# Kernel tuning notes

Hardware: AMD Instinct MI355X
Metric: run time of the kernel (lower is better)

Reference implementation:

```python
import jax, jax.numpy as jnp
import numpy as np

KPS = 39
EPS = 1e-05

def _prelu(h, a):
    return jnp.where(h >= 0, h, a * h)

def _ln(h, alpha, beta):
    mean = jnp.mean(h, axis=-1, keepdims=True)
    var = jnp.mean((h - mean) ** 2, axis=-1, keepdims=True)
    return (h - mean) / jnp.sqrt(var + EPS) * alpha + beta

def setup_inputs() -> dict:
    key = jax.random.key(0)
    ks = jax.random.split(key, 8)
    B, T = 256, 2048
    d_in, d_hid = 2 * KPS, 5 * KPS  # 78, 195
    # xavier_uniform with gain for relu = sqrt(2)
    def xavier(k, shape):
        fan_out, fan_in = shape
        gain = np.sqrt(2.0)
        bound = gain * np.sqrt(6.0 / (fan_in + fan_out))
        return jax.random.uniform(k, shape, jnp.float32, -bound, bound)
    return {
        "x": jax.random.normal(ks[0], (B, T, KPS), jnp.float32),
        "y": jax.random.normal(ks[1], (B, T, KPS), jnp.float32),
        "W1": xavier(ks[2], (d_hid, d_in)),   # [195, 78]
        "b1": jnp.zeros((d_hid,), jnp.float32),
        "W2": xavier(ks[3], (d_in, d_hid)),   # [78, 195]
        "b2": jnp.zeros((d_in,), jnp.float32),
        "a1": jnp.full((1,), 0.25, jnp.float32),  # PReLU default
        "a2": jnp.full((1,), 0.25, jnp.float32),
        "alpha1": jnp.ones((d_hid,), jnp.float32),
        "beta1": jnp.zeros((d_hid,), jnp.float32),
        "alpha2": jnp.ones((d_in,), jnp.float32),
        "beta2": jnp.zeros((d_in,), jnp.float32),
    }

def reference(x, y, W1, b1, W2, b2, a1, a2, alpha1, beta1, alpha2, beta2):
    joined = jnp.concatenate((x, y), axis=-1)        # [B, T, 78]
    h = jnp.einsum('btd,hd->bth', joined, W1) + b1   # [B, T, 195]
    h = _ln(_prelu(h, a1), alpha1, beta1)
    # dropout p=0.1 is identity in eval mode
    h = jnp.einsum('bth,dh->btd', h, W2) + b2        # [B, T, 78]
    h = _ln(_prelu(h, a2), alpha2, beta2)
    out = h + joined
    return out[..., :KPS], out[..., KPS:]
```

## Files before the change

kernel.cpp:

```cpp
#include <hip/hip_runtime.h>
#include <hip/hip_bf16.h>

typedef unsigned short u16;
typedef unsigned int   u32;

#define KPS     39
#define DIN     78
#define DHID    195
#define NTOKTOT (256*2048)

#define S1      104
#define S2      232
#define M1T     13
#define K1S     3
#define M2T     5
#define K2S     7
#define NW      8
#define TPI     (NW*16)
#define TPB     2048
#define NIT     (TPB/TPI)
#define NBLK    (NTOKTOT/TPB)

#define W1F_E (M1T*K1S*64*8)
#define W2F_E (M2T*K2S*64*8)
#define JND_E (TPI*S1)
#define HN_E  (TPI*S2)
#define SMEM_BYTES ((W1F_E+W2F_E+JND_E+HN_E)*2 + DIN*2*4 + DIN*4)

typedef __attribute__((ext_vector_type(8))) short short8;
typedef __attribute__((ext_vector_type(4))) float float4v;

static __device__ __forceinline__ u16 f2b(float v) {
  __hip_bfloat16 b = __float2bfloat16(v);
  return __builtin_bit_cast(u16, b);
}
static __device__ __forceinline__ float b2f(u16 u) {
  return __builtin_bit_cast(float, ((u32)u) << 16);
}

extern "C" __global__ __launch_bounds__(512, 2)
void fused_mlp_kernel(const float* __restrict__ xp,  const float* __restrict__ yp,
                      const float* __restrict__ W1p, const float* __restrict__ b1p,
                      const float* __restrict__ W2p, const float* __restrict__ b2p,
                      const float* __restrict__ a1p, const float* __restrict__ a2p,
                      const float* __restrict__ al1p,const float* __restrict__ be1p,
                      const float* __restrict__ al2p,const float* __restrict__ be2p,
                      float* __restrict__ out0, float* __restrict__ out1)
{
  extern __shared__ char smem[];
  u16*   W1F = (u16*)smem;
  u16*   W2F = W1F + W1F_E;
  u16*   JND = W2F + W2F_E;
  u16*   HN  = JND + JND_E;
  float* AB2 = (float*)(HN + HN_E);
  float* B2C = AB2 + DIN*2;

  const int tid  = threadIdx.x;
  const int lane = tid & 63;
  const int w    = tid >> 6;
  const int c    = lane & 15;
  const int quad = lane >> 4;
  const int wr   = w * 16;
  const int blockTok = blockIdx.x * TPB;

  float4v xr0, xr1, xr2, yr0, yr1, yr2;
  {
    const float4v* xw = (const float4v*)(xp + (size_t)(blockTok + wr) * KPS);
    const float4v* yw = (const float4v*)(yp + (size_t)(blockTok + wr) * KPS);
    xr0 = xw[lane];      yr0 = yw[lane];
    xr1 = xw[lane + 64]; yr1 = yw[lane + 64];
    if (lane < 28) { xr2 = xw[lane + 128]; yr2 = yw[lane + 128]; }
    else { xr2 = (float4v)0.f; yr2 = (float4v)0.f; }
  }

  {
    float* SCR = (float*)JND;
    if (tid < DIN*4) {
      int d = tid >> 2, p = tid & 3;
      float s = (p == 0) ? b2p[d] : 0.f;
      const float* wrow = W2p + d*DHID;
      for (int j = p; j < DHID; j += 4) s = __builtin_fmaf(wrow[j], be1p[j], s);
      SCR[tid] = s;
    }
  }
  __syncthreads();
  if (tid < DIN) {
    const float* SCR = (const float*)JND;
    B2C[tid] = SCR[4*tid] + SCR[4*tid+1] + SCR[4*tid+2] + SCR[4*tid+3];
    AB2[2*tid+0] = al2p[tid];
    AB2[2*tid+1] = be2p[tid];
  }
  for (int s = tid; s < M1T*K1S*64; s += 512) {
    int m = s/(K1S*64), r = s - m*(K1S*64);
    int kt = r >> 6, l = r & 63;
    int cc = l & 15, qq = l >> 4;
    int row = m*16 + cc, k0 = kt*32 + qq*8;
    short8 v;
    #pragma unroll
    for (int e = 0; e < 8; ++e) {
      int k = k0 + e; float f = 0.f;
      if (row < DHID) { if (k < DIN) f = W1p[row*DIN + k]; else if (k == DIN) f = b1p[row]; }
      v[e] = (short)f2b(f);
    }
    *(short8*)&W1F[(size_t)s*8] = v;
  }
  __syncthreads();
  for (int s = tid; s < M2T*K2S*64; s += 512) {
    int m = s/(K2S*64), r = s - m*(K2S*64);
    int kt = r >> 6, l = r & 63;
    int cc = l & 15, qq = l >> 4;
    int d = m*16 + cc, k0 = kt*32 + qq*8;
    short8 v;
    #pragma unroll
    for (int e = 0; e < 8; ++e) {
      int k = k0 + e; float f = 0.f;
      if (d < DIN) {
        if (k < DHID)       f = W2p[d*DHID + k] * al1p[k];
        else if (k == DHID) f = B2C[d];
      }
      v[e] = (short)f2b(f);
    }
    *(short8*)&W2F[(size_t)s*8] = v;
  }
  for (int i = tid; i < TPI*18; i += 512) {
    int t = i/18, cf = i - t*18;
    JND[t*S1 + DIN + cf] = (cf == 0) ? (u16)0x3F80 : (u16)0;
  }
  for (int i = tid; i < TPI*29; i += 512) {
    int t = i/29, cf = i - t*29;
    HN[t*S2 + DHID + cf] = (cf == 0) ? (u16)0x3F80 : (u16)0;
  }
  __syncthreads();

  const float a1v = a1p[0];
  const float a2v = a2p[0];

  int joff[12];
  #pragma unroll
  for (int s = 0; s < 3; ++s) {
    int i4 = lane + s*64;
    #pragma unroll
    for (int k = 0; k < 4; ++k) {
      int idx = i4*4 + k;
      int t = idx / KPS, cc2 = idx - t*KPS;
      joff[s*4+k] = (wr + t)*S1 + cc2;
    }
  }

  const u16* pW1 = W1F + (size_t)lane*8;
  const u16* pW2 = W2F + (size_t)lane*8;
  u16* pJ = JND + (wr + c)*S1;
  u16* pH = HN  + (wr + c)*S2;

  #pragma unroll 1
  for (int it = 0; it < NIT; ++it) {
    const int tb = blockTok + it * TPI;

    #pragma unroll
    for (int k = 0; k < 4; ++k) {
      JND[joff[k]]         = f2b(xr0[k]);
      JND[joff[k] + KPS]   = f2b(yr0[k]);
      JND[joff[4+k]]       = f2b(xr1[k]);
      JND[joff[4+k] + KPS] = f2b(yr1[k]);
    }
    if (lane < 28) {
      #pragma unroll
      for (int k = 0; k < 4; ++k) {
        JND[joff[8+k]]       = f2b(xr2[k]);
        JND[joff[8+k] + KPS] = f2b(yr2[k]);
      }
    }

    if (it + 1 < NIT) {
      const float4v* xw = (const float4v*)(xp + (size_t)(tb + TPI + wr) * KPS);
      const float4v* yw = (const float4v*)(yp + (size_t)(tb + TPI + wr) * KPS);
      xr0 = xw[lane];      yr0 = yw[lane];
      xr1 = xw[lane + 64]; yr1 = yw[lane + 64];
      if (lane < 28) { xr2 = xw[lane + 128]; yr2 = yw[lane + 128]; }
    }

    float4v acc1[M1T];
    #pragma unroll
    for (int m = 0; m < M1T; ++m)
      #pragma unroll
      for (int q = 0; q < 4; ++q) acc1[m][q] = 0.f;

    #pragma unroll
    for (int kt = 0; kt < K1S; ++kt) {
      short8 bfr = *(const short8*)&pJ[kt*32 + quad*8];
      #pragma unroll
      for (int m = 0; m < M1T; ++m) {
        short8 afr = *(const short8*)&pW1[(m*K1S + kt)*512];
        acc1[m] = __builtin_amdgcn_mfma_f32_16x16x32_bf16(afr, bfr, acc1[m], 0, 0, 0);
      }
    }

    float sum = 0.f, ss = 0.f;
    #pragma unroll
    for (int m = 0; m < M1T; ++m)
      #pragma unroll
      for (int q = 0; q < 4; ++q) {
        float h = acc1[m][q];
        float p = fmaxf(h, 0.f) + a1v * fminf(h, 0.f);
        acc1[m][q] = p;
        sum += p;
        ss = __builtin_fmaf(p, p, ss);
      }
    sum += __shfl_xor(sum, 16, 64);
    sum += __shfl_xor(sum, 32, 64);
    ss  += __shfl_xor(ss,  16, 64);
    ss  += __shfl_xor(ss,  32, 64);
    const float mean = sum * (1.f/DHID);
    const float istd = rsqrtf(ss*(1.f/DHID) - mean*mean + 1e-5f);

    #pragma unroll
    for (int m = 0; m < M1T; ++m) {
      int jb = m*16 + quad*4;
      if (m < 12) {
        ushort4 pk;
        pk.x = f2b((acc1[m][0] - mean)*istd);
        pk.y = f2b((acc1[m][1] - mean)*istd);
        pk.z = f2b((acc1[m][2] - mean)*istd);
        pk.w = f2b((acc1[m][3] - mean)*istd);
        *(ushort4*)&pH[jb] = pk;
      } else if (quad == 0) {
        pH[192] = f2b((acc1[m][0] - mean)*istd);
        pH[193] = f2b((acc1[m][1] - mean)*istd);
        pH[194] = f2b((acc1[m][2] - mean)*istd);
      }
    }

    float4v acc2[M2T];
    #pragma unroll
    for (int m = 0; m < M2T; ++m)
      #pragma unroll
      for (int q = 0; q < 4; ++q) acc2[m][q] = 0.f;

    #pragma unroll
    for (int kt = 0; kt < K2S; ++kt) {
      short8 bfr = *(const short8*)&pH[kt*32 + quad*8];
      #pragma unroll
      for (int m = 0; m < M2T; ++m) {
        short8 afr = *(const short8*)&pW2[(m*K2S + kt)*512];
        acc2[m] = __builtin_amdgcn_mfma_f32_16x16x32_bf16(afr, bfr, acc2[m], 0, 0, 0);
      }
    }

    float sum2 = 0.f, ss2 = 0.f;
    #pragma unroll
    for (int m = 0; m < M2T; ++m)
      #pragma unroll
      for (int q = 0; q < 4; ++q) {
        float h = acc2[m][q];
        float p = fmaxf(h, 0.f) + a2v * fminf(h, 0.f);
        acc2[m][q] = p;
        sum2 += p;
        ss2 = __builtin_fmaf(p, p, ss2);
      }
    sum2 += __shfl_xor(sum2, 16, 64);
    sum2 += __shfl_xor(sum2, 32, 64);
    ss2  += __shfl_xor(ss2,  16, 64);
    ss2  += __shfl_xor(ss2,  32, 64);
    const float mean2 = sum2 * (1.f/DIN);
    const float istd2 = rsqrtf(ss2*(1.f/DIN) - mean2*mean2 + 1e-5f);

    const int gt = tb + wr + c;
    #pragma unroll
    for (int m = 0; m < M2T; ++m) {
      int d0 = m*16 + quad*4;
      if (d0 < DIN) {
        ushort4 res = *(const ushort4*)&pJ[d0];
        u16 rr[4] = {res.x, res.y, res.z, res.w};
        #pragma unroll
        for (int r = 0; r < 4; ++r) {
          int d = d0 + r;
          if (d < DIN) {
            float2 ab = *(const float2*)&AB2[2*d];
            float  v  = (acc2[m][r] - mean2)*istd2*ab.x + ab.y + b2f(rr[r]);
            if (d < KPS) out0[(size_t)gt*KPS + d]         = v;
            else         out1[(size_t)gt*KPS + (d - KPS)] = v;
          }
        }
      }
    }
  }
}

extern "C" void kernel_launch(void* const* d_in, const int* in_sizes, int n_in,
                              void* d_out, int out_size, void* d_ws, size_t ws_size,
                              hipStream_t stream) {
  const float* xp   = (const float*)d_in[0];
  const float* yp   = (const float*)d_in[1];
  const float* W1p  = (const float*)d_in[2];
  const float* b1p  = (const float*)d_in[3];
  const float* W2p  = (const float*)d_in[4];
  const float* b2p  = (const float*)d_in[5];
  const float* a1p  = (const float*)d_in[6];
  const float* a2p  = (const float*)d_in[7];
  const float* al1p = (const float*)d_in[8];
  const float* be1p = (const float*)d_in[9];
  const float* al2p = (const float*)d_in[10];
  const float* be2p = (const float*)d_in[11];

  float* out0 = (float*)d_out;
  float* out1 = out0 + (size_t)NTOKTOT * KPS;

  hipFuncSetAttribute((const void*)fused_mlp_kernel,
                      hipFuncAttributeMaxDynamicSharedMemorySize, SMEM_BYTES);

  fused_mlp_kernel<<<NBLK, 512, SMEM_BYTES, stream>>>(
      xp, yp, W1p, b1p, W2p, b2p, a1p, a2p, al1p, be1p, al2p, be2p, out0, out1);
}
```

Measured before the change: 363.1 us.

## Feed GEMM2 B operand from registers, drop HN LDS buffer, double warps

Removes the HN shared-memory staging of the normalized hidden activations. The W2 fragment layout is permuted along K so the MFMA accumulator output of GEMM1 can be packed directly in registers as the B operand of GEMM2, saving an LDS write/read round trip per iteration. The freed LDS is used to raise the block from 8 to 16 waves (1024 threads) with launch bounds of 4. This raises occupancy but may increase register pressure from the packed array, and the preamble and synchronization now span a larger block.

```diff
diff --git a/kernel.cpp b/kernel.cpp
--- a/kernel.cpp
+++ b/kernel.cpp
@@ -10,12 +10,12 @@
 #define NTOKTOT (256*2048)
 
 #define S1      104
-#define S2      232
 #define M1T     13
 #define K1S     3
 #define M2T     5
 #define K2S     7
-#define NW      8
+#define NW      16
+#define NTHR    1024
 #define TPI     (NW*16)
 #define TPB     2048
 #define NIT     (TPB/TPI)
@@ -24,11 +24,11 @@
 #define W1F_E (M1T*K1S*64*8)
 #define W2F_E (M2T*K2S*64*8)
 #define JND_E (TPI*S1)
-#define HN_E  (TPI*S2)
-#define SMEM_BYTES ((W1F_E+W2F_E+JND_E+HN_E)*2 + DIN*2*4 + DIN*4)
+#define SMEM_BYTES ((W1F_E+W2F_E+JND_E)*2 + DIN*2*4 + DIN*4)
 
 typedef __attribute__((ext_vector_type(8))) short short8;
 typedef __attribute__((ext_vector_type(4))) float float4v;
+typedef __attribute__((ext_vector_type(4))) u32   uint4v;
 
 static __device__ __forceinline__ u16 f2b(float v) {
   __hip_bfloat16 b = __float2bfloat16(v);
@@ -38,7 +38,7 @@
   return __builtin_bit_cast(float, ((u32)u) << 16);
 }
 
-extern "C" __global__ __launch_bounds__(512, 2)
+extern "C" __global__ __launch_bounds__(NTHR, 4)
 void fused_mlp_kernel(const float* __restrict__ xp,  const float* __restrict__ yp,
                       const float* __restrict__ W1p, const float* __restrict__ b1p,
                       const float* __restrict__ W2p, const float* __restrict__ b2p,
@@ -51,8 +51,7 @@
   u16*   W1F = (u16*)smem;
   u16*   W2F = W1F + W1F_E;
   u16*   JND = W2F + W2F_E;
-  u16*   HN  = JND + JND_E;
-  float* AB2 = (float*)(HN + HN_E);
+  float* AB2 = (float*)(JND + JND_E);
   float* B2C = AB2 + DIN*2;
 
   const int tid  = threadIdx.x;
@@ -90,7 +89,7 @@
     AB2[2*tid+0] = al2p[tid];
     AB2[2*tid+1] = be2p[tid];
   }
-  for (int s = tid; s < M1T*K1S*64; s += 512) {
+  for (int s = tid; s < M1T*K1S*64; s += NTHR) {
     int m = s/(K1S*64), r = s - m*(K1S*64);
     int kt = r >> 6, l = r & 63;
     int cc = l & 15, qq = l >> 4;
@@ -105,15 +104,16 @@
     *(short8*)&W1F[(size_t)s*8] = v;
   }
   __syncthreads();
-  for (int s = tid; s < M2T*K2S*64; s += 512) {
+  for (int s = tid; s < M2T*K2S*64; s += NTHR) {
     int m = s/(K2S*64), r = s - m*(K2S*64);
     int kt = r >> 6, l = r & 63;
     int cc = l & 15, qq = l >> 4;
-    int d = m*16 + cc, k0 = kt*32 + qq*8;
+    int d = m*16 + cc;
     short8 v;
     #pragma unroll
     for (int e = 0; e < 8; ++e) {
-      int k = k0 + e; float f = 0.f;
+      int k = kt*32 + (e>>2)*16 + qq*4 + (e&3);
+      float f = 0.f;
       if (d < DIN) {
         if (k < DHID)       f = W2p[d*DHID + k] * al1p[k];
         else if (k == DHID) f = B2C[d];
@@ -122,13 +122,9 @@
     }
     *(short8*)&W2F[(size_t)s*8] = v;
   }
-  for (int i = tid; i < TPI*18; i += 512) {
+  for (int i = tid; i < TPI*18; i += NTHR) {
     int t = i/18, cf = i - t*18;
     JND[t*S1 + DIN + cf] = (cf == 0) ? (u16)0x3F80 : (u16)0;
-  }
-  for (int i = tid; i < TPI*29; i += 512) {
-    int t = i/29, cf = i - t*29;
-    HN[t*S2 + DHID + cf] = (cf == 0) ? (u16)0x3F80 : (u16)0;
   }
   __syncthreads();
 
@@ -150,7 +146,6 @@
   const u16* pW1 = W1F + (size_t)lane*8;
   const u16* pW2 = W2F + (size_t)lane*8;
   u16* pJ = JND + (wr + c)*S1;
-  u16* pH = HN  + (wr + c)*S2;
 
   #pragma unroll 1
   for (int it = 0; it < NIT; ++it) {
@@ -213,21 +208,23 @@
     const float mean = sum * (1.f/DHID);
     const float istd = rsqrtf(ss*(1.f/DHID) - mean*mean + 1e-5f);
 
-    #pragma unroll
-    for (int m = 0; m < M1T; ++m) {
-      int jb = m*16 + quad*4;
-      if (m < 12) {
-        ushort4 pk;
-        pk.x = f2b((acc1[m][0] - mean)*istd);
-        pk.y = f2b((acc1[m][1] - mean)*istd);
-        pk.z = f2b((acc1[m][2] - mean)*istd);
-        pk.w = f2b((acc1[m][3] - mean)*istd);
-        *(ushort4*)&pH[jb] = pk;
-      } else if (quad == 0) {
-        pH[192] = f2b((acc1[m][0] - mean)*istd);
-        pH[193] = f2b((acc1[m][1] - mean)*istd);
-        pH[194] = f2b((acc1[m][2] - mean)*istd);
-      }
+    u32 pn[26];
+    #pragma unroll
+    for (int m = 0; m < 12; ++m) {
+      u16 p0 = f2b((acc1[m][0] - mean)*istd);
+      u16 p1 = f2b((acc1[m][1] - mean)*istd);
+      u16 p2 = f2b((acc1[m][2] - mean)*istd);
+      u16 p3 = f2b((acc1[m][3] - mean)*istd);
+      pn[2*m]   = (u32)p0 | ((u32)p1 << 16);
+      pn[2*m+1] = (u32)p2 | ((u32)p3 << 16);
+    }
+    {
+      float n0 = (quad == 0) ? (acc1[12][0] - mean)*istd : 0.f;
+      float n1 = (quad == 0) ? (acc1[12][1] - mean)*istd : 0.f;
+      float n2 = (quad == 0) ? (acc1[12][2] - mean)*istd : 0.f;
+      u16 pb = (quad == 0) ? (u16)0x3F80 : (u16)0;
+      pn[24] = (u32)f2b(n0) | ((u32)f2b(n1) << 16);
+      pn[25] = (u32)f2b(n2) | ((u32)pb    << 16);
     }
 
     float4v acc2[M2T];
@@ -238,7 +235,12 @@
 
     #pragma unroll
     for (int kt = 0; kt < K2S; ++kt) {
-      short8 bfr = *(const short8*)&pH[kt*32 + quad*8];
+      uint4v bu;
+      bu[0] = pn[4*kt + 0];
+      bu[1] = pn[4*kt + 1];
+      bu[2] = (kt < 6) ? pn[4*kt + 2] : 0u;
+      bu[3] = (kt < 6) ? pn[4*kt + 3] : 0u;
+      short8 bfr = __builtin_bit_cast(short8, bu);
       #pragma unroll
       for (int m = 0; m < M2T; ++m) {
         short8 afr = *(const short8*)&pW2[(m*K2S + kt)*512];
@@ -308,6 +310,6 @@
   hipFuncSetAttribute((const void*)fused_mlp_kernel,
                       hipFuncAttributeMaxDynamicSharedMemorySize, SMEM_BYTES);
 
-  fused_mlp_kernel<<<NBLK, 512, SMEM_BYTES, stream>>>(
+  fused_mlp_kernel<<<NBLK, NTHR, SMEM_BYTES, stream>>>(
       xp, yp, W1p, b1p, W2p, b2p, a1p, a2p, al1p, be1p, al2p, be2p, out0, out1);
 }
```

After: 452.9 us. +24.7%, slower.
